# Kernel tuning notes

Measured on AMD Instinct MI355X. Metric: run time of the kernel, lower is better.

The kernel has to match this reference:

```python
import jax, jax.numpy as jnp
import numpy as np
import math

def _eq_conv1x1(x, w):
    # EqualizedConv2d: 1x1 conv, no bias, weight scaled by sqrt(2 / fan_in) at runtime.
    scale = math.sqrt(2.0 / w.shape[1])
    return jnp.einsum('bchw,oc->bohw', x, w * scale)

def _maxpool2x2(x):
    b, c, h, w = x.shape
    return x.reshape(b, c, h // 2, 2, w // 2, 2).max(axis=(3, 5))

def setup_inputs() -> dict:
    key = jax.random.key(0)
    ks = jax.random.split(key, 6)
    B, Cin, H, W = 8, 256, 64, 64
    Cout = 512
    return {
        'x': jax.random.normal(ks[0], (B, Cin, H, W), dtype=jnp.float32),
        'w_theta': jax.random.normal(ks[1], (Cout // 8, Cin), dtype=jnp.float32),
        'w_phi': jax.random.normal(ks[2], (Cout // 8, Cin), dtype=jnp.float32),
        'w_g': jax.random.normal(ks[3], (Cout // 2, Cin), dtype=jnp.float32),
        'w_o': jax.random.normal(ks[4], (Cout, Cout // 2), dtype=jnp.float32),
        'w_res': jax.random.normal(ks[5], (Cout, Cin), dtype=jnp.float32),
        'gamma': jnp.ones((1,), dtype=jnp.float32),
    }

def reference(x, w_theta, w_phi, w_g, w_o, w_res, gamma):
    B, _, H, W = x.shape
    theta = _eq_conv1x1(x, w_theta).reshape(B, -1, H * W)          # [B, Co/8, HW]
    phi = _maxpool2x2(_eq_conv1x1(x, w_phi)).reshape(B, -1, H * W // 4)  # [B, Co/8, HW/4]
    g = _maxpool2x2(_eq_conv1x1(x, w_g)).reshape(B, -1, H * W // 4)      # [B, Co/2, HW/4]
    # attention: softmax over key dim (no 1/sqrt(d) scaling, as in the original)
    scores = jnp.einsum('bcn,bcm->bnm', theta, phi)                # [B, HW, HW/4]
    beta = jax.nn.softmax(scores, axis=-1)
    att = jnp.einsum('bcm,bnm->bcn', g, beta).reshape(B, -1, H, W)  # [B, Co/2, H, W]
    out = _eq_conv1x1(att, w_o)                                     # [B, Co, H, W]
    res = _eq_conv1x1(x, w_res)
    inv_sqrt2 = jnp.float32(1.0 / math.sqrt(2.0))
    return (gamma[0] * out + res) * inv_sqrt2
```

## Files before the change

### kernel.cpp

```cpp
#include <hip/hip_runtime.h>


typedef _Float16 f16;
typedef f16 f16x2 __attribute__((ext_vector_type(2)));
typedef f16 f16x4 __attribute__((ext_vector_type(4)));
typedef f16 f16x8 __attribute__((ext_vector_type(8)));
typedef float f32x4 __attribute__((ext_vector_type(4)));

#define MFMA16(a, b, c) __builtin_amdgcn_mfma_f32_16x16x32_f16((a), (b), (c), 0, 0, 0)

__device__ __forceinline__ void gload16(const void* src, void* dst_lds) {
  __builtin_amdgcn_global_load_lds(
      (const __attribute__((address_space(1))) void*)src,
      (__attribute__((address_space(3))) void*)dst_lds, 16, 0, 0);
}

__global__ __launch_bounds__(256, 4)
void k_prep_w(const float* __restrict__ wt, const float* __restrict__ wp,
              const float* __restrict__ wg, const float* __restrict__ wo,
              const float* __restrict__ wr, const float* __restrict__ gamma,
              f16* __restrict__ Wproj, f16* __restrict__ Wcat) {
  int i = blockIdx.x * 256 + threadIdx.x;
  const float s = 0.08838834764831845f;
  const float is2 = 0.7071067811865476f;
  if (i < 384 * 256) {
    float v = (i < 64 * 256) ? wt[i]
              : (i < 128 * 256 ? wp[i - 64 * 256] : wg[i - 128 * 256]);
    Wproj[i] = (f16)(v * s);
  } else {
    int j = i - 384 * 256;
    if (j < 512 * 512) {
      int r = j >> 9, c = j & 511;
      float v = (c < 256) ? wo[r * 256 + c] * (gamma[0] * s * is2)
                          : wr[r * 256 + (c - 256)] * (s * is2);
      Wcat[j] = (f16)v;
    }
  }
}

__global__ __launch_bounds__(256, 4)
void k_transpose(const float* __restrict__ x, f16* __restrict__ xT) {
  __shared__ f16 tile[64 * 72];
  int b = blockIdx.z, nt = blockIdx.y, ct = blockIdx.x;
  int t = threadIdx.x;
  {
    int c = t >> 2, nch = (t & 3) * 16;
    const float* src = x + (((size_t)b * 256 + ct * 64 + c) << 12) + nt * 64 + nch;
    float4 v0 = *(const float4*)(src);
    float4 v1 = *(const float4*)(src + 4);
    float4 v2 = *(const float4*)(src + 8);
    float4 v3 = *(const float4*)(src + 12);
    f16x8 a = {(f16)v0.x, (f16)v0.y, (f16)v0.z, (f16)v0.w,
               (f16)v1.x, (f16)v1.y, (f16)v1.z, (f16)v1.w};
    f16x8 bb = {(f16)v2.x, (f16)v2.y, (f16)v2.z, (f16)v2.w,
                (f16)v3.x, (f16)v3.y, (f16)v3.z, (f16)v3.w};
    *(f16x8*)&tile[c * 72 + nch] = a;
    *(f16x8*)&tile[c * 72 + nch + 8] = bb;
  }
  __syncthreads();
  {
    int n = t >> 2, cch = (t & 3) * 16;
    f16 tmp[16];
#pragma unroll
    for (int i = 0; i < 16; i++) tmp[i] = tile[(cch + i) * 72 + n];
    f16x8 a, bb;
#pragma unroll
    for (int i = 0; i < 8; i++) { a[i] = tmp[i]; bb[i] = tmp[8 + i]; }
    f16* dst = xT + (((size_t)b * 4096 + nt * 64 + n) << 8) + ct * 64 + cch;
    *(f16x8*)dst = a;
    *(f16x8*)(dst + 8) = bb;
  }
}

__global__ __launch_bounds__(256, 2)
void k_gemm_projq(const f16* __restrict__ xT, const f16* __restrict__ Wproj,
                  f16* __restrict__ Q, f16* __restrict__ Kp, f16* __restrict__ V) {
  __shared__ f16 lds[192 * 64];
  f16* Alds = lds;
  f16* Blds = lds + 64 * 64;
  int b = blockIdx.z, mt = blockIdx.y, nt = blockIdx.x;
  int tid = threadIdx.x;
  int lane = tid & 63, wave = tid >> 6;
  int wm = wave >> 1, wn = wave & 1;
  int l15 = lane & 15, hi = lane >> 4;
  f32x4 acc[2][4];
#pragma unroll
  for (int mf = 0; mf < 2; mf++)
#pragma unroll
    for (int nf = 0; nf < 4; nf++) acc[mf][nf] = (f32x4){0, 0, 0, 0};
  const f16* Abase = Wproj + ((mt * 64) << 8);
  const f16* Bbase = xT + (((size_t)b * 4096 + nt * 128) << 8);
  for (int k0 = 0; k0 < 256; k0 += 64) {
    __syncthreads();
#pragma unroll
    for (int i = 0; i < 2; i++) {
      int chunk = i * 256 + tid;
      int row = chunk >> 3, cc = chunk & 7, scc = cc ^ (row & 7);
      gload16(Abase + (row << 8) + k0 + scc * 8, (char*)Alds + (i * 256 + wave * 64) * 16);
    }
#pragma unroll
    for (int i = 0; i < 4; i++) {
      int chunk = i * 256 + tid;
      int row = chunk >> 3, cc = chunk & 7, scc = cc ^ (row & 7);
      gload16(Bbase + (row << 8) + k0 + scc * 8, (char*)Blds + (i * 256 + wave * 64) * 16);
    }
    __syncthreads();
#pragma unroll
    for (int ks = 0; ks < 2; ks++) {
      int cb = (hi * 8 + ks * 32) * 2;
      f16x8 af[2], bf[4];
#pragma unroll
      for (int mf = 0; mf < 2; mf++) {
        int row = wm * 32 + mf * 16 + l15;
        af[mf] = *(const f16x8*)((const char*)Alds + row * 128 + (cb ^ ((row & 7) << 4)));
      }
#pragma unroll
      for (int nf = 0; nf < 4; nf++) {
        int row = wn * 64 + nf * 16 + l15;
        bf[nf] = *(const f16x8*)((const char*)Blds + row * 128 + (cb ^ ((row & 7) << 4)));
      }
#pragma unroll
      for (int mf = 0; mf < 2; mf++)
#pragma unroll
        for (int nf = 0; nf < 4; nf++) acc[mf][nf] = MFMA16(af[mf], bf[nf], acc[mf][nf]);
    }
  }
  if (mt == 0) {
#pragma unroll
    for (int mf = 0; mf < 2; mf++)
#pragma unroll
      for (int nf = 0; nf < 4; nf++)
#pragma unroll
        for (int r = 0; r < 4; r++) {
          int jl = wm * 32 + mf * 16 + hi * 4 + r;
          int n = nt * 128 + wn * 64 + nf * 16 + l15;
          Q[(((size_t)b * 4096 + n) << 6) + jl] = (f16)acc[mf][nf][r];
        }
  } else {
    __syncthreads();
    f16* Pool = lds;
#pragma unroll
    for (int mf = 0; mf < 2; mf++)
#pragma unroll
      for (int nf = 0; nf < 4; nf++)
#pragma unroll
        for (int r = 0; r < 4; r++) {
          int jl = wm * 32 + mf * 16 + hi * 4 + r;
          int col = wn * 64 + nf * 16 + l15;
          Pool[jl * 132 + col] = (f16)acc[mf][nf][r];
        }
    __syncthreads();
    if (mt == 1) {
      int m_l = tid >> 3;
      int jj8 = (tid & 7) * 8;
      f16x8 w;
#pragma unroll
      for (int i = 0; i < 8; i++) {
        int jj = jj8 + i;
        f16x2 p0 = *(const f16x2*)&Pool[jj * 132 + 2 * m_l];
        f16x2 p1 = *(const f16x2*)&Pool[jj * 132 + 64 + 2 * m_l];
        float v = fmaxf(fmaxf((float)p0[0], (float)p0[1]),
                        fmaxf((float)p1[0], (float)p1[1]));
        w[i] = (f16)v;
      }
      *(f16x8*)&Kp[((size_t)b * 1024 + nt * 32 + m_l) * 64 + jj8] = w;
    } else {
      int ch_l = tid >> 2;
      int m8 = (tid & 3) * 8;
      f16x8 w;
#pragma unroll
      for (int i = 0; i < 8; i++) {
        int mm = m8 + i;
        f16x2 p0 = *(const f16x2*)&Pool[ch_l * 132 + 2 * mm];
        f16x2 p1 = *(const f16x2*)&Pool[ch_l * 132 + 64 + 2 * mm];
        float v = fmaxf(fmaxf((float)p0[0], (float)p0[1]),
                        fmaxf((float)p1[0], (float)p1[1]));
        w[i] = (f16)v;
      }
      int ch = (mt - 2) * 64 + ch_l;
      *(f16x8*)&V[(((size_t)b * 256 + ch) << 10) + nt * 32 + m8] = w;
    }
  }
}

__global__ __launch_bounds__(512, 2)
void k_flash(const f16* __restrict__ Q, const f16* __restrict__ Kp,
             const f16* __restrict__ V, f16* __restrict__ att) {
  __shared__ f16 Klds[2][64 * 64];
  __shared__ f16 Vlds[2][256 * 64];
  __shared__ f16 Plds[8][32 * 72];
  int b = blockIdx.y, qt = blockIdx.x;
  int tid = threadIdx.x;
  int lane = tid & 63, wave = tid >> 6;
  int rg = wave >> 1, cg2 = wave & 1;
  int l15 = lane & 15, hi = lane >> 4;
  const f16* Kb = Kp + ((size_t)b << 16);
  const f16* Vb = V + ((size_t)b << 18);
  f16* Pw = &Plds[wave][0];
  const float L2E = 1.44269504f;
  f16x8 qf[2][2];
#pragma unroll
  for (int h = 0; h < 2; h++)
#pragma unroll
    for (int ks = 0; ks < 2; ks++)
      qf[h][ks] = *(const f16x8*)(
          Q + (((size_t)b * 4096 + qt * 128 + rg * 32 + h * 16 + l15) << 6) +
          ks * 32 + hi * 8);
  f32x4 o[2][8];
#pragma unroll
  for (int h = 0; h < 2; h++)
#pragma unroll
    for (int i = 0; i < 8; i++) o[h][i] = (f32x4){0, 0, 0, 0};
  float mrow[2] = {-1e30f, -1e30f};
  float lrow[2] = {0.f, 0.f};

  int cbase = hi * 16;

#define STAGE(bufi, kt)                                                          \
  {                                                                              \
    {                                                                            \
      int chunk = tid;                                                           \
      int row = chunk >> 3, cc = chunk & 7, scc = cc ^ (row & 7);                \
      gload16(Kb + (((kt) * 64 + row) << 6) + scc * 8,                           \
              (char*)&Klds[bufi][0] + chunk * 16);                               \
    }                                                                            \
    _Pragma("unroll") for (int i = 0; i < 4; i++) {                              \
      int chunk = i * 512 + tid;                                                 \
      int row = chunk >> 3, cc = chunk & 7, scc = cc ^ (row & 7);                \
      gload16(Vb + ((size_t)row << 10) + (kt) * 64 + scc * 8,                    \
              (char*)&Vlds[bufi][0] + chunk * 16);                               \
    }                                                                            \
  }

  STAGE(0, 0);
  __syncthreads();
  int buf = 0;
  for (int kt = 0; kt < 16; ++kt) {
    if (kt < 15) STAGE(buf ^ 1, kt + 1);
    f32x4 s[2][4];
#pragma unroll
    for (int h = 0; h < 2; h++)
#pragma unroll
      for (int mf = 0; mf < 4; mf++) s[h][mf] = (f32x4){0, 0, 0, 0};
#pragma unroll
    for (int ks = 0; ks < 2; ks++) {
      f16x8 kf[4];
#pragma unroll
      for (int mf = 0; mf < 4; mf++) {
        int row = mf * 16 + l15;
        kf[mf] = *(const f16x8*)((const char*)&Klds[buf][0] + row * 128 +
                                 ((cbase + ks * 64) ^ ((row & 7) << 4)));
      }
#pragma unroll
      for (int h = 0; h < 2; h++)
#pragma unroll
        for (int mf = 0; mf < 4; mf++)
          s[h][mf] = MFMA16(kf[mf], qf[h][ks], s[h][mf]);
    }
    float pmax[2];
#pragma unroll
    for (int h = 0; h < 2; h++) {
      float t0 = fmaxf(fmaxf(s[h][0][0], s[h][1][0]), fmaxf(s[h][2][0], s[h][3][0]));
      float t1 = fmaxf(fmaxf(s[h][0][1], s[h][1][1]), fmaxf(s[h][2][1], s[h][3][1]));
      float t2 = fmaxf(fmaxf(s[h][0][2], s[h][1][2]), fmaxf(s[h][2][2], s[h][3][2]));
      float t3 = fmaxf(fmaxf(s[h][0][3], s[h][1][3]), fmaxf(s[h][2][3], s[h][3][3]));
      float mx = fmaxf(fmaxf(t0, t1), fmaxf(t2, t3));
      mx = fmaxf(mx, __shfl_xor(mx, 16, 64));
      mx = fmaxf(mx, __shfl_xor(mx, 32, 64));
      pmax[h] = mx;
    }
    bool need = (pmax[0] > mrow[0] + 8.f) || (pmax[1] > mrow[1] + 8.f);
    if (__any(need)) {
#pragma unroll
      for (int h = 0; h < 2; h++) {
        float mnew = fmaxf(mrow[h], pmax[h]);
        float corr = __builtin_amdgcn_exp2f((mrow[h] - mnew) * L2E);
        lrow[h] *= corr;
        mrow[h] = mnew;
#pragma unroll
        for (int r = 0; r < 4; r++) {
          float cr = __shfl(corr, (hi << 4) + (hi << 2) + r, 64);
#pragma unroll
          for (int cf = 0; cf < 8; cf++) o[h][cf][r] *= cr;
        }
      }
    }
#pragma unroll
    for (int h = 0; h < 2; h++) {
      float e[4][4];
#pragma unroll
      for (int mf = 0; mf < 4; mf++)
#pragma unroll
        for (int r = 0; r < 4; r++)
          e[mf][r] = __builtin_amdgcn_exp2f((s[h][mf][r] - mrow[h]) * L2E);
#pragma unroll
      for (int mf = 0; mf < 4; mf++) {
        f16x4 w = {(f16)e[mf][0], (f16)e[mf][1], (f16)e[mf][2], (f16)e[mf][3]};
        *(f16x4*)((char*)Pw + (h * 16 + l15) * 144 + mf * 32 + hi * 8) = w;
      }
      float u0 = (e[0][0] + e[1][0]) + (e[2][0] + e[3][0]);
      float u1 = (e[0][1] + e[1][1]) + (e[2][1] + e[3][1]);
      float u2 = (e[0][2] + e[1][2]) + (e[2][2] + e[3][2]);
      float u3 = (e[0][3] + e[1][3]) + (e[2][3] + e[3][3]);
      float sum = (u0 + u1) + (u2 + u3);
      sum += __shfl_xor(sum, 16, 64);
      sum += __shfl_xor(sum, 32, 64);
      lrow[h] += sum;
    }
#pragma unroll
    for (int ks = 0; ks < 2; ks++) {
      f16x8 af[2];
#pragma unroll
      for (int h = 0; h < 2; h++)
        af[h] = *(const f16x8*)((char*)Pw + (h * 16 + l15) * 144 + ks * 64 + hi * 16);
      __builtin_amdgcn_s_setprio(1);
#pragma unroll
      for (int cg = 0; cg < 2; cg++) {
        f16x8 vf[4];
#pragma unroll
        for (int u = 0; u < 4; u++) {
          int row = (cg2 * 8 + cg * 4 + u) * 16 + l15;
          vf[u] = *(const f16x8*)((const char*)&Vlds[buf][0] + row * 128 +
                                  ((cbase + ks * 64) ^ ((row & 7) << 4)));
        }
#pragma unroll
        for (int h = 0; h < 2; h++)
#pragma unroll
          for (int u = 0; u < 4; u++)
            o[h][cg * 4 + u] = MFMA16(af[h], vf[u], o[h][cg * 4 + u]);
      }
      __builtin_amdgcn_s_setprio(0);
    }
    __syncthreads();
    buf ^= 1;
  }
#undef STAGE
  int nbase = qt * 128 + rg * 32 + hi * 4;
#pragma unroll
  for (int h = 0; h < 2; h++) {
    float inv = 1.f / lrow[h];
#pragma unroll
    for (int r = 0; r < 4; r++) {
      float iv = __shfl(inv, (hi << 4) + (hi << 2) + r, 64);
#pragma unroll
      for (int cf = 0; cf < 8; cf++) {
        int n = nbase + h * 16 + r;
        int c = cg2 * 128 + cf * 16 + l15;
        att[(((size_t)b * 4096 + n) << 8) + c] = (f16)(o[h][cf][r] * iv);
      }
    }
  }
}

__global__ __launch_bounds__(256, 2)
void k_gemm_out(const f16* __restrict__ Wcat, const f16* __restrict__ att,
                const f16* __restrict__ xT, float* __restrict__ out) {
  __shared__ f16 Alds[128 * 64];
  __shared__ f16 Blds[128 * 64];
  int b = blockIdx.z, mt = blockIdx.y, nt = blockIdx.x;
  int lane = threadIdx.x & 63, wave = threadIdx.x >> 6;
  int wm = wave >> 1, wn = wave & 1;
  f32x4 acc[4][4];
#pragma unroll
  for (int mf = 0; mf < 4; mf++)
#pragma unroll
    for (int nf = 0; nf < 4; nf++) acc[mf][nf] = (f32x4){0, 0, 0, 0};
  const f16* Abase = Wcat + (size_t)(mt * 128) * 512;
  for (int k0 = 0; k0 < 512; k0 += 64) {
    __syncthreads();
#pragma unroll
    for (int i = 0; i < 4; i++) {
      int chunk = i * 256 + threadIdx.x;
      int row = chunk >> 3, cc = chunk & 7, scc = cc ^ (row & 7);
      gload16(Abase + row * 512 + k0 + scc * 8, (char*)Alds + (i * 256 + wave * 64) * 16);
    }
    const f16* Bcol = (k0 < 256) ? (att + (((size_t)b * 4096 + nt * 128) << 8))
                                 : (xT + (((size_t)b * 4096 + nt * 128) << 8));
    int kk = (k0 < 256) ? k0 : (k0 - 256);
#pragma unroll
    for (int i = 0; i < 4; i++) {
      int chunk = i * 256 + threadIdx.x;
      int row = chunk >> 3, cc = chunk & 7, scc = cc ^ (row & 7);
      gload16(Bcol + (row << 8) + kk + scc * 8, (char*)Blds + (i * 256 + wave * 64) * 16);
    }
    __syncthreads();
#pragma unroll
    for (int ks = 0; ks < 2; ks++) {
      int cb = ((lane >> 4) * 8 + ks * 32) * 2;
      f16x8 af[4], bf[4];
#pragma unroll
      for (int mf = 0; mf < 4; mf++) {
        int row = wm * 64 + mf * 16 + (lane & 15);
        af[mf] = *(const f16x8*)((const char*)Alds + row * 128 + (cb ^ ((row & 7) << 4)));
      }
#pragma unroll
      for (int nf = 0; nf < 4; nf++) {
        int row = wn * 64 + nf * 16 + (lane & 15);
        bf[nf] = *(const f16x8*)((const char*)Blds + row * 128 + (cb ^ ((row & 7) << 4)));
      }
#pragma unroll
      for (int mf = 0; mf < 4; mf++)
#pragma unroll
        for (int nf = 0; nf < 4; nf++) acc[mf][nf] = MFMA16(af[mf], bf[nf], acc[mf][nf]);
    }
  }
#pragma unroll
  for (int mf = 0; mf < 4; mf++)
#pragma unroll
    for (int nf = 0; nf < 4; nf++)
#pragma unroll
      for (int r = 0; r < 4; r++) {
        int oo = mt * 128 + wm * 64 + mf * 16 + (lane >> 4) * 4 + r;
        int n = nt * 128 + wn * 64 + nf * 16 + (lane & 15);
        out[(((size_t)b * 512 + oo) << 12) + n] = acc[mf][nf][r];
      }
}

extern "C" void kernel_launch(void* const* d_in, const int* in_sizes, int n_in,
                              void* d_out, int out_size, void* d_ws, size_t ws_size,
                              hipStream_t stream) {
  const float* x = (const float*)d_in[0];
  const float* wt = (const float*)d_in[1];
  const float* wp = (const float*)d_in[2];
  const float* wg = (const float*)d_in[3];
  const float* wo = (const float*)d_in[4];
  const float* wr = (const float*)d_in[5];
  const float* gm = (const float*)d_in[6];
  float* out = (float*)d_out;
  char* ws = (char*)d_ws;
  const size_t MB = 1024 * 1024;
  f16* xT = (f16*)(ws);
  f16* Qb = (f16*)(ws + 16 * MB);
  f16* Kp = (f16*)(ws + 20 * MB);
  f16* Vb = (f16*)(ws + 21 * MB);
  f16* Wproj = (f16*)(ws + 25 * MB);
  f16* Wcat = (f16*)(ws + 25 * MB + 512 * 1024);
  f16* att = (f16*)(ws + 26 * MB);

  hipLaunchKernelGGL(k_prep_w, dim3(1408), dim3(256), 0, stream, wt, wp, wg, wo, wr, gm,
                     Wproj, Wcat);
  hipLaunchKernelGGL(k_transpose, dim3(4, 64, 8), dim3(256), 0, stream, x, xT);
  hipLaunchKernelGGL(k_gemm_projq, dim3(32, 6, 8), dim3(256), 0, stream, xT, Wproj, Qb,
                     Kp, Vb);
  hipLaunchKernelGGL(k_flash, dim3(32, 8), dim3(512), 0, stream, Qb, Kp, Vb, att);
  hipLaunchKernelGGL(k_gemm_out, dim3(32, 4, 8), dim3(256), 0, stream, Wcat, att, xT, out);
}
```

Measured before the change: 107.7 us.

## Halve flash query tile, single-buffer K/V to raise occupancy and grid size

The flash-attention kernel now handles 64 query rows per block instead of 128, with each wave owning 16 rows, and the grid doubles to 512 blocks. K/V LDS staging drops from double-buffered to single-buffered with two barriers per tile, and the launch bound asks for 4 blocks per CU. This spreads work across more CUs and cuts registers and LDS per block. In exchange it gives up overlap of loads with compute, adds a barrier per iteration, and loads each K/V tile twice as often in total.

```diff
diff --git a/kernel.cpp b/kernel.cpp
--- a/kernel.cpp
+++ b/kernel.cpp
@@ -183,12 +183,12 @@
   }
 }
 
-__global__ __launch_bounds__(512, 2)
+__global__ __launch_bounds__(512, 4)
 void k_flash(const f16* __restrict__ Q, const f16* __restrict__ Kp,
              const f16* __restrict__ V, f16* __restrict__ att) {
-  __shared__ f16 Klds[2][64 * 64];
-  __shared__ f16 Vlds[2][256 * 64];
-  __shared__ f16 Plds[8][32 * 72];
+  __shared__ f16 Klds[64 * 64];
+  __shared__ f16 Vlds[256 * 64];
+  __shared__ f16 Plds[8][16 * 72];
   int b = blockIdx.y, qt = blockIdx.x;
   int tid = threadIdx.x;
   int lane = tid & 63, wave = tid >> 6;
@@ -198,105 +198,82 @@
   const f16* Vb = V + ((size_t)b << 18);
   f16* Pw = &Plds[wave][0];
   const float L2E = 1.44269504f;
-  f16x8 qf[2][2];
-#pragma unroll
-  for (int h = 0; h < 2; h++)
-#pragma unroll
-    for (int ks = 0; ks < 2; ks++)
-      qf[h][ks] = *(const f16x8*)(
-          Q + (((size_t)b * 4096 + qt * 128 + rg * 32 + h * 16 + l15) << 6) +
-          ks * 32 + hi * 8);
-  f32x4 o[2][8];
-#pragma unroll
-  for (int h = 0; h < 2; h++)
-#pragma unroll
-    for (int i = 0; i < 8; i++) o[h][i] = (f32x4){0, 0, 0, 0};
-  float mrow[2] = {-1e30f, -1e30f};
-  float lrow[2] = {0.f, 0.f};
+  f16x8 qf[2];
+#pragma unroll
+  for (int ks = 0; ks < 2; ks++)
+    qf[ks] = *(const f16x8*)(
+        Q + (((size_t)b * 4096 + qt * 64 + rg * 16 + l15) << 6) + ks * 32 + hi * 8);
+  f32x4 o[8];
+#pragma unroll
+  for (int i = 0; i < 8; i++) o[i] = (f32x4){0, 0, 0, 0};
+  float mrow = -1e30f, lrow = 0.f;
 
   int cbase = hi * 16;
 
-#define STAGE(bufi, kt)                                                          \
+#define STAGE(kt)                                                                \
   {                                                                              \
     {                                                                            \
       int chunk = tid;                                                           \
       int row = chunk >> 3, cc = chunk & 7, scc = cc ^ (row & 7);                \
       gload16(Kb + (((kt) * 64 + row) << 6) + scc * 8,                           \
-              (char*)&Klds[bufi][0] + chunk * 16);                               \
+              (char*)&Klds[0] + chunk * 16);                                     \
     }                                                                            \
     _Pragma("unroll") for (int i = 0; i < 4; i++) {                              \
       int chunk = i * 512 + tid;                                                 \
       int row = chunk >> 3, cc = chunk & 7, scc = cc ^ (row & 7);                \
       gload16(Vb + ((size_t)row << 10) + (kt) * 64 + scc * 8,                    \
-              (char*)&Vlds[bufi][0] + chunk * 16);                               \
+              (char*)&Vlds[0] + chunk * 16);                                     \
     }                                                                            \
   }
 
-  STAGE(0, 0);
+  STAGE(0);
   __syncthreads();
-  int buf = 0;
   for (int kt = 0; kt < 16; ++kt) {
-    if (kt < 15) STAGE(buf ^ 1, kt + 1);
-    f32x4 s[2][4];
-#pragma unroll
-    for (int h = 0; h < 2; h++)
-#pragma unroll
-      for (int mf = 0; mf < 4; mf++) s[h][mf] = (f32x4){0, 0, 0, 0};
+    f32x4 s[4];
+#pragma unroll
+    for (int mf = 0; mf < 4; mf++) s[mf] = (f32x4){0, 0, 0, 0};
 #pragma unroll
     for (int ks = 0; ks < 2; ks++) {
       f16x8 kf[4];
 #pragma unroll
       for (int mf = 0; mf < 4; mf++) {
         int row = mf * 16 + l15;
-        kf[mf] = *(const f16x8*)((const char*)&Klds[buf][0] + row * 128 +
+        kf[mf] = *(const f16x8*)((const char*)&Klds[0] + row * 128 +
                                  ((cbase + ks * 64) ^ ((row & 7) << 4)));
       }
 #pragma unroll
-      for (int h = 0; h < 2; h++)
-#pragma unroll
-        for (int mf = 0; mf < 4; mf++)
-          s[h][mf] = MFMA16(kf[mf], qf[h][ks], s[h][mf]);
-    }
-    float pmax[2];
-#pragma unroll
-    for (int h = 0; h < 2; h++) {
-      float t0 = fmaxf(fmaxf(s[h][0][0], s[h][1][0]), fmaxf(s[h][2][0], s[h][3][0]));
-      float t1 = fmaxf(fmaxf(s[h][0][1], s[h][1][1]), fmaxf(s[h][2][1], s[h][3][1]));
-      float t2 = fmaxf(fmaxf(s[h][0][2], s[h][1][2]), fmaxf(s[h][2][2], s[h][3][2]));
-      float t3 = fmaxf(fmaxf(s[h][0][3], s[h][1][3]), fmaxf(s[h][2][3], s[h][3][3]));
-      float mx = fmaxf(fmaxf(t0, t1), fmaxf(t2, t3));
-      mx = fmaxf(mx, __shfl_xor(mx, 16, 64));
-      mx = fmaxf(mx, __shfl_xor(mx, 32, 64));
-      pmax[h] = mx;
-    }
-    bool need = (pmax[0] > mrow[0] + 8.f) || (pmax[1] > mrow[1] + 8.f);
-    if (__any(need)) {
-#pragma unroll
-      for (int h = 0; h < 2; h++) {
-        float mnew = fmaxf(mrow[h], pmax[h]);
-        float corr = __builtin_amdgcn_exp2f((mrow[h] - mnew) * L2E);
-        lrow[h] *= corr;
-        mrow[h] = mnew;
-#pragma unroll
-        for (int r = 0; r < 4; r++) {
-          float cr = __shfl(corr, (hi << 4) + (hi << 2) + r, 64);
-#pragma unroll
-          for (int cf = 0; cf < 8; cf++) o[h][cf][r] *= cr;
-        }
-      }
-    }
-#pragma unroll
-    for (int h = 0; h < 2; h++) {
+      for (int mf = 0; mf < 4; mf++) s[mf] = MFMA16(kf[mf], qf[ks], s[mf]);
+    }
+    float t0 = fmaxf(fmaxf(s[0][0], s[1][0]), fmaxf(s[2][0], s[3][0]));
+    float t1 = fmaxf(fmaxf(s[0][1], s[1][1]), fmaxf(s[2][1], s[3][1]));
+    float t2 = fmaxf(fmaxf(s[0][2], s[1][2]), fmaxf(s[2][2], s[3][2]));
+    float t3 = fmaxf(fmaxf(s[0][3], s[1][3]), fmaxf(s[2][3], s[3][3]));
+    float mx = fmaxf(fmaxf(t0, t1), fmaxf(t2, t3));
+    mx = fmaxf(mx, __shfl_xor(mx, 16, 64));
+    mx = fmaxf(mx, __shfl_xor(mx, 32, 64));
+    if (__any(mx > mrow + 8.f)) {
+      float mnew = fmaxf(mrow, mx);
+      float corr = __builtin_amdgcn_exp2f((mrow - mnew) * L2E);
+      lrow *= corr;
+      mrow = mnew;
+#pragma unroll
+      for (int r = 0; r < 4; r++) {
+        float cr = __shfl(corr, (hi << 4) + (hi << 2) + r, 64);
+#pragma unroll
+        for (int cf = 0; cf < 8; cf++) o[cf][r] *= cr;
+      }
+    }
+    {
       float e[4][4];
 #pragma unroll
       for (int mf = 0; mf < 4; mf++)
 #pragma unroll
         for (int r = 0; r < 4; r++)
-          e[mf][r] = __builtin_amdgcn_exp2f((s[h][mf][r] - mrow[h]) * L2E);
+          e[mf][r] = __builtin_amdgcn_exp2f((s[mf][r] - mrow) * L2E);
 #pragma unroll
       for (int mf = 0; mf < 4; mf++) {
         f16x4 w = {(f16)e[mf][0], (f16)e[mf][1], (f16)e[mf][2], (f16)e[mf][3]};
-        *(f16x4*)((char*)Pw + (h * 16 + l15) * 144 + mf * 32 + hi * 8) = w;
+        *(f16x4*)((char*)Pw + l15 * 144 + mf * 32 + hi * 8) = w;
       }
       float u0 = (e[0][0] + e[1][0]) + (e[2][0] + e[3][0]);
       float u1 = (e[0][1] + e[1][1]) + (e[2][1] + e[3][1]);
@@ -305,14 +282,11 @@
       float sum = (u0 + u1) + (u2 + u3);
       sum += __shfl_xor(sum, 16, 64);
       sum += __shfl_xor(sum, 32, 64);
-      lrow[h] += sum;
+      lrow += sum;
     }
 #pragma unroll
     for (int ks = 0; ks < 2; ks++) {
-      f16x8 af[2];
-#pragma unroll
-      for (int h = 0; h < 2; h++)
-        af[h] = *(const f16x8*)((char*)Pw + (h * 16 + l15) * 144 + ks * 64 + hi * 16);
+      f16x8 af = *(const f16x8*)((char*)Pw + l15 * 144 + ks * 64 + hi * 16);
       __builtin_amdgcn_s_setprio(1);
 #pragma unroll
       for (int cg = 0; cg < 2; cg++) {
@@ -320,34 +294,31 @@
 #pragma unroll
         for (int u = 0; u < 4; u++) {
           int row = (cg2 * 8 + cg * 4 + u) * 16 + l15;
-          vf[u] = *(const f16x8*)((const char*)&Vlds[buf][0] + row * 128 +
+          vf[u] = *(const f16x8*)((const char*)&Vlds[0] + row * 128 +
                                   ((cbase + ks * 64) ^ ((row & 7) << 4)));
         }
 #pragma unroll
-        for (int h = 0; h < 2; h++)
-#pragma unroll
-          for (int u = 0; u < 4; u++)
-            o[h][cg * 4 + u] = MFMA16(af[h], vf[u], o[h][cg * 4 + u]);
+        for (int u = 0; u < 4; u++) o[cg * 4 + u] = MFMA16(af, vf[u], o[cg * 4 + u]);
       }
       __builtin_amdgcn_s_setprio(0);
     }
-    __syncthreads();
-    buf ^= 1;
+    if (kt < 15) {
+      __syncthreads();
+      STAGE(kt + 1);
+      __syncthreads();
+    }
   }
 #undef STAGE
-  int nbase = qt * 128 + rg * 32 + hi * 4;
-#pragma unroll
-  for (int h = 0; h < 2; h++) {
-    float inv = 1.f / lrow[h];
-#pragma unroll
-    for (int r = 0; r < 4; r++) {
-      float iv = __shfl(inv, (hi << 4) + (hi << 2) + r, 64);
-#pragma unroll
-      for (int cf = 0; cf < 8; cf++) {
-        int n = nbase + h * 16 + r;
-        int c = cg2 * 128 + cf * 16 + l15;
-        att[(((size_t)b * 4096 + n) << 8) + c] = (f16)(o[h][cf][r] * iv);
-      }
+  int nbase = qt * 64 + rg * 16 + hi * 4;
+  float inv = 1.f / lrow;
+#pragma unroll
+  for (int r = 0; r < 4; r++) {
+    float iv = __shfl(inv, (hi << 4) + (hi << 2) + r, 64);
+#pragma unroll
+    for (int cf = 0; cf < 8; cf++) {
+      int n = nbase + r;
+      int c = cg2 * 128 + cf * 16 + l15;
+      att[(((size_t)b * 4096 + n) << 8) + c] = (f16)(o[cf][r] * iv);
     }
   }
 }
@@ -442,6 +413,6 @@
   hipLaunchKernelGGL(k_transpose, dim3(4, 64, 8), dim3(256), 0, stream, x, xT);
   hipLaunchKernelGGL(k_gemm_projq, dim3(32, 6, 8), dim3(256), 0, stream, xT, Wproj, Qb,
                      Kp, Vb);
-  hipLaunchKernelGGL(k_flash, dim3(32, 8), dim3(512), 0, stream, Qb, Kp, Vb, att);
+  hipLaunchKernelGGL(k_flash, dim3(64, 8), dim3(512), 0, stream, Qb, Kp, Vb, att);
   hipLaunchKernelGGL(k_gemm_out, dim3(32, 4, 8), dim3(256), 0, stream, Wcat, att, xT, out);
 }
```

New measurement: 108.8 us. About the same (+1.0%).
